# Kernel tuning notes

Measured on AMD Instinct MI355X. Metric: run time of the kernel, lower is better.

## Reference

```python
import jax, jax.numpy as jnp
import numpy as np
from math import sqrt

B, S, D, H = 2, 2048, 1024, 16
HD = D // H


def setup_inputs() -> dict:
    key = jax.random.key(0)
    ks = jax.random.split(key, 5)
    std = 0.02
    return {
        "tensor_in": jax.random.normal(ks[0], (B, S, D), dtype=jnp.float32),
        "attention_mask": jnp.zeros((1, 1, S, S), dtype=jnp.float32),
        "Wq": jax.random.normal(ks[1], (D, D), dtype=jnp.float32) * std,
        "Wk": jax.random.normal(ks[2], (D, D), dtype=jnp.float32) * std,
        "Wv": jax.random.normal(ks[3], (D, D), dtype=jnp.float32) * std,
        "Wo": jax.random.normal(ks[4], (D, D), dtype=jnp.float32) * std,
    }


def reference(tensor_in, attention_mask, Wq, Wk, Wv, Wo):
    # nn.Linear(dim, dim, bias=False): y = x @ W.T, W is [out, in]
    q = tensor_in @ Wq.T  # [B,S,D]
    k = tensor_in @ Wk.T
    v = tensor_in @ Wv.T
    # split heads -> [B,H,S,HD]
    q = q.reshape(B, S, H, HD).transpose(0, 2, 1, 3)
    k = k.reshape(B, S, H, HD).transpose(0, 2, 1, 3)
    v = v.reshape(B, S, H, HD).transpose(0, 2, 1, 3)
    # scores [B,H,S,S]; note: mask added BEFORE scaling, scale = sqrt(full dim)
    scores = jnp.einsum("bhqd,bhkd->bhqk", q, k) + attention_mask
    weights = jax.nn.softmax(scores / sqrt(D), axis=-1)  # dropout = identity (eval)
    context = jnp.einsum("bhqk,bhkd->bhqd", weights, v)
    context = context.transpose(0, 2, 1, 3).reshape(B, S, D)
    return context @ Wo.T
```

## Files before the change

kernel.cpp:

```cpp
#include <hip/hip_runtime.h>

#define B_  2
#define S_  2048
#define D_  1024
#define H_  16
#define HD_ 64
#define M_  (B_*S_)

typedef __attribute__((ext_vector_type(8))) short  short8;
typedef __attribute__((ext_vector_type(4))) float  float4v;
typedef __attribute__((ext_vector_type(4))) int    int4v;

#define PSCALE 0.0450843341f

__device__ __forceinline__ unsigned int pack2_bf16(float a, float b) {
#if __has_builtin(__builtin_amdgcn_cvt_pk_bf16_f32)
    auto p = __builtin_amdgcn_cvt_pk_bf16_f32(a, b);
    return __builtin_bit_cast(unsigned int, p);
#else
    unsigned int xa = __builtin_bit_cast(unsigned int, a);
    unsigned int xb = __builtin_bit_cast(unsigned int, b);
    xa += 0x7fffu + ((xa >> 16) & 1u);
    xb += 0x7fffu + ((xb >> 16) & 1u);
    return (xa >> 16) | (xb & 0xffff0000u);
#endif
}
__device__ __forceinline__ unsigned short f_to_bf16bits(float f) {
#if __has_builtin(__builtin_amdgcn_cvt_pk_bf16_f32)
    return (unsigned short)(pack2_bf16(f, f) & 0xffffu);
#else
    unsigned int x = __builtin_bit_cast(unsigned int, f);
    x += 0x7fffu + ((x >> 16) & 1u);
    return (unsigned short)(x >> 16);
#endif
}

__device__ __forceinline__ float fast_exp2(float x) {
#if __has_builtin(__builtin_amdgcn_exp2f)
    return __builtin_amdgcn_exp2f(x);
#else
    return exp2f(x);
#endif
}

__device__ __forceinline__ void async_cp16(const unsigned short* gsrc,
                                           unsigned short* lds_base_uniform) {
#if __has_builtin(__builtin_amdgcn_global_load_lds)
    __builtin_amdgcn_global_load_lds(
        (const __attribute__((address_space(1))) unsigned int*)gsrc,
        (__attribute__((address_space(3))) unsigned int*)lds_base_uniform,
        16, 0, 0);
#else
    const int lane = (int)(threadIdx.x & 63);
    *(int4v*)(lds_base_uniform + lane * 8) = *(const int4v*)gsrc;
#endif
}

__global__ __launch_bounds__(256) void cvt_bf16(
    const float* __restrict__ X,  const float* __restrict__ Wq,
    const float* __restrict__ Wk, const float* __restrict__ Wv,
    const float* __restrict__ Wo,
    unsigned short* __restrict__ Xb,  unsigned short* __restrict__ Wqb,
    unsigned short* __restrict__ Wkb, unsigned short* __restrict__ Wvb,
    unsigned short* __restrict__ Wob)
{
    const long t = (long)blockIdx.x * 256 + threadIdx.x;
    const long e = t * 8;
    const float* src; unsigned short* dst; long off;
    if      (e < 4194304) { src = X;  dst = Xb;  off = e; }
    else if (e < 5242880) { src = Wq; dst = Wqb; off = e - 4194304; }
    else if (e < 6291456) { src = Wk; dst = Wkb; off = e - 5242880; }
    else if (e < 7340032) { src = Wv; dst = Wvb; off = e - 6291456; }
    else                  { src = Wo; dst = Wob; off = e - 7340032; }
    float4v a = *(const float4v*)&src[off];
    float4v b = *(const float4v*)&src[off + 4];
    int4v o;
    o[0] = (int)pack2_bf16(a[0], a[1]);
    o[1] = (int)pack2_bf16(a[2], a[3]);
    o[2] = (int)pack2_bf16(b[0], b[1]);
    o[3] = (int)pack2_bf16(b[2], b[3]);
    *(int4v*)&dst[off] = o;
}

__global__ __launch_bounds__(256) void gemm_bt(
    const unsigned short* __restrict__ A,
    const unsigned short* __restrict__ B0,
    const unsigned short* __restrict__ B1,
    const unsigned short* __restrict__ B2,
    void* __restrict__ O0, void* __restrict__ O1, void* __restrict__ O2,
    int mode_base)
{
    const int K = 1024;
    const int z = blockIdx.z;
    const int mode = mode_base + z;
    const unsigned short* Aop;
    const unsigned short* Bop;
    void* Op = (z == 0) ? O0 : (z == 1) ? O1 : O2;
    int m0, n0;
    if (mode == 2) {
        Aop = B2; Bop = A;
        m0 = blockIdx.y * 128;
        n0 = blockIdx.x * 128;
    } else {
        Aop = A;
        Bop = (z == 0) ? B0 : (z == 1) ? B1 : B2;
        m0 = blockIdx.x * 128;
        n0 = blockIdx.y * 128;
    }

    __shared__ alignas(16) unsigned short As[128 * 64];
    __shared__ alignas(16) unsigned short Bs[128 * 64];

    const int tid  = threadIdx.x;
    const int wv   = tid >> 6;
    const int lane = tid & 63;
    const int wm   = wv >> 1, wn = wv & 1;
    const int q4   = lane >> 4, l15 = lane & 15;

    const unsigned short* gA[4];
    const unsigned short* gB[4];
    unsigned short* ldsA[4];
    unsigned short* ldsB[4];
#pragma unroll
    for (int j = 0; j < 4; j++) {
        const int r = wv * 32 + j * 8 + (lane >> 3);
        const int c = (((lane & 7) ^ (r & 7)) * 8);
        gA[j] = Aop + (long)(m0 + r) * K + c;
        gB[j] = Bop + (long)(n0 + r) * K + c;
        ldsA[j] = &As[(wv * 32 + j * 8) * 64];
        ldsB[j] = &Bs[(wv * 32 + j * 8) * 64];
    }

    int aoff[2][4], boff[2][4];
#pragma unroll
    for (int ks = 0; ks < 2; ks++)
#pragma unroll
        for (int t = 0; t < 4; t++) {
            const int swz = (((ks * 4 + q4) ^ (l15 & 7)) * 8);
            aoff[ks][t] = (wm * 64 + t * 16 + l15) * 64 + swz;
            boff[ks][t] = (wn * 64 + t * 16 + l15) * 64 + swz;
        }

    float4v acc[4][4];
#pragma unroll
    for (int i = 0; i < 4; i++)
#pragma unroll
        for (int j = 0; j < 4; j++) acc[i][j] = (float4v)0.0f;

    for (int k0 = 0; k0 < K; k0 += 64) {
        __syncthreads();
#pragma unroll
        for (int j = 0; j < 4; j++) {
            async_cp16(gA[j], ldsA[j]);
            async_cp16(gB[j], ldsB[j]);
            gA[j] += 64; gB[j] += 64;
        }
        __syncthreads();

#pragma unroll
        for (int ks = 0; ks < 2; ks++) {
            short8 afr[4], bfr[4];
#pragma unroll
            for (int mt = 0; mt < 4; mt++) afr[mt] = *(const short8*)&As[aoff[ks][mt]];
#pragma unroll
            for (int nt = 0; nt < 4; nt++) bfr[nt] = *(const short8*)&Bs[boff[ks][nt]];
#pragma unroll
            for (int mt = 0; mt < 4; mt++)
#pragma unroll
                for (int nt = 0; nt < 4; nt++)
                    acc[mt][nt] = __builtin_amdgcn_mfma_f32_16x16x32_bf16(
                        afr[mt], bfr[nt], acc[mt][nt], 0, 0, 0);
        }
    }

#pragma unroll
    for (int mt = 0; mt < 4; mt++)
#pragma unroll
        for (int nt = 0; nt < 4; nt++)
#pragma unroll
            for (int r = 0; r < 4; r++) {
                const int m = m0 + wm * 64 + mt * 16 + q4 * 4 + r;
                const int n = n0 + wn * 64 + nt * 16 + l15;
                float v = acc[mt][nt][r];
                if (mode == 3) {
                    ((float*)Op)[(long)m * D_ + n] = v;
                } else if (mode == 2) {
                    const long off = (((long)(n >> 11) * H_ + (m >> 6)) * HD_ + (m & 63)) * S_ + (n & 2047);
                    ((unsigned short*)Op)[off] = f_to_bf16bits(v);
                } else {
                    const long off = ((long)((m >> 11) * H_ + (n >> 6)) * S_ + (m & 2047)) * HD_ + (n & 63);
                    if (mode == 0) v *= PSCALE;
                    ((unsigned short*)Op)[off] = f_to_bf16bits(v);
                }
            }
}

__global__ __launch_bounds__(512, 4) void attn(
    const unsigned short* __restrict__ Q,
    const unsigned short* __restrict__ Kk,
    const unsigned short* __restrict__ Vt,
    const float* __restrict__ mask,
    unsigned short* __restrict__ ctx)
{
    __shared__ alignas(16) unsigned short Ks [2][64 * 72];
    __shared__ alignas(16) unsigned short Vts[2][64 * 72];
    __shared__ alignas(16) unsigned short Ps [8][16 * 72];

    const int tid  = threadIdx.x;
    const int wv   = tid >> 6;
    const int lane = tid & 63;
    const int q4   = lane >> 4, l15 = lane & 15;
    const int bh   = blockIdx.y;
    const int q0   = blockIdx.x * 128;

    const long head = (long)bh * S_ * HD_;

    const int qrow = q0 + wv * 16 + l15;
    short8 qfr[2];
    qfr[0] = *(const short8*)&Q[head + (long)qrow * HD_ + q4 * 8];
    qfr[1] = *(const short8*)&Q[head + (long)qrow * HD_ + 32 + q4 * 8];

    float l_acc[4] = {0.0f, 0.0f, 0.0f, 0.0f};
    float4v oacc[4];
#pragma unroll
    for (int dt = 0; dt < 4; dt++) oacc[dt] = (float4v)0.0f;

    const int srow = tid >> 3;
    const int scol = (tid & 7) * 8;
    const unsigned short* gK = Kk + head + (long)srow * HD_ + scol;
    const unsigned short* gV = Vt + head + (long)srow * S_  + scol;
    const int ldsOff = srow * 72 + scol;

    const float* mrow[4];
#pragma unroll
    for (int r = 0; r < 4; r++)
        mrow[r] = mask + (long)(q0 + wv * 16 + q4 * 4 + r) * S_ + l15;

    int4v kreg = *(const int4v*)gK;
    int4v vreg = *(const int4v*)gV;

    for (int it = 0; it < S_ / 64; it++) {
        const int k0  = it * 64;
        const int buf = it & 1;

        *(int4v*)&Ks [buf][ldsOff] = kreg;
        *(int4v*)&Vts[buf][ldsOff] = vreg;
        __syncthreads();

        if (it + 1 < S_ / 64) {
            kreg = *(const int4v*)(gK + (long)(k0 + 64) * HD_);
            vreg = *(const int4v*)(gV + (k0 + 64));
        }

        float mv[4][4];
#pragma unroll
        for (int nt = 0; nt < 4; nt++)
#pragma unroll
            for (int r = 0; r < 4; r++)
                mv[nt][r] = mrow[r][k0 + nt * 16];

        float4v sfr[4];
#pragma unroll
        for (int nt = 0; nt < 4; nt++) {
            short8 kb0 = *(const short8*)&Ks[buf][(nt * 16 + l15) * 72 + q4 * 8];
            short8 kb1 = *(const short8*)&Ks[buf][(nt * 16 + l15) * 72 + 32 + q4 * 8];
            float4v s = (float4v)0.0f;
            s = __builtin_amdgcn_mfma_f32_16x16x32_bf16(qfr[0], kb0, s, 0, 0, 0);
            s = __builtin_amdgcn_mfma_f32_16x16x32_bf16(qfr[1], kb1, s, 0, 0, 0);
            sfr[nt] = s;
        }

#pragma unroll
        for (int nt = 0; nt < 4; nt++)
#pragma unroll
            for (int r = 0; r < 4; r++) {
                const float p = fast_exp2(fmaf(mv[nt][r], PSCALE, sfr[nt][r]));
                l_acc[r] += p;
                Ps[wv][(q4 * 4 + r) * 72 + nt * 16 + l15] = f_to_bf16bits(p);
            }

        short8 pf0 = *(const short8*)&Ps[wv][l15 * 72 + q4 * 8];
        short8 pf1 = *(const short8*)&Ps[wv][l15 * 72 + 32 + q4 * 8];

#pragma unroll
        for (int dt = 0; dt < 4; dt++) {
            short8 vb0 = *(const short8*)&Vts[buf][(dt * 16 + l15) * 72 + q4 * 8];
            short8 vb1 = *(const short8*)&Vts[buf][(dt * 16 + l15) * 72 + 32 + q4 * 8];
            float4v o = oacc[dt];
            o = __builtin_amdgcn_mfma_f32_16x16x32_bf16(pf0, vb0, o, 0, 0, 0);
            o = __builtin_amdgcn_mfma_f32_16x16x32_bf16(pf1, vb1, o, 0, 0, 0);
            oacc[dt] = o;
        }
    }

#pragma unroll
    for (int r = 0; r < 4; r++) {
#pragma unroll
        for (int off = 1; off < 16; off <<= 1)
            l_acc[r] += __shfl_xor(l_acc[r], off);
    }

    const int b = bh >> 4, h = bh & 15;
#pragma unroll
    for (int dt = 0; dt < 4; dt++)
#pragma unroll
        for (int r = 0; r < 4; r++) {
            const int qg = q0 + wv * 16 + q4 * 4 + r;
            const int d  = dt * 16 + l15;
            const float v = oacc[dt][r] / l_acc[r];
            ctx[((long)(b * S_ + qg)) * D_ + h * HD_ + d] = f_to_bf16bits(v);
        }
}

extern "C" void kernel_launch(void* const* d_in, const int* in_sizes, int n_in,
                              void* d_out, int out_size, void* d_ws, size_t ws_size,
                              hipStream_t stream) {
    const float* X    = (const float*)d_in[0];
    const float* mask = (const float*)d_in[1];
    const float* Wq   = (const float*)d_in[2];
    const float* Wk   = (const float*)d_in[3];
    const float* Wv   = (const float*)d_in[4];
    const float* Wo   = (const float*)d_in[5];
    float* out        = (float*)d_out;

    unsigned short* ws = (unsigned short*)d_ws;
    unsigned short* qws  = ws;
    unsigned short* kws  = ws + 4194304;
    unsigned short* vtws = ws + 8388608;
    unsigned short* ctx  = ws + 12582912;
    unsigned short* Xb   = ws + 16777216;
    unsigned short* Wqb  = ws + 20971520;
    unsigned short* Wkb  = ws + 22020096;
    unsigned short* Wvb  = ws + 23068672;
    unsigned short* Wob  = ws + 24117248;

    cvt_bf16<<<dim3(4096), 256, 0, stream>>>(X, Wq, Wk, Wv, Wo, Xb, Wqb, Wkb, Wvb, Wob);
    gemm_bt<<<dim3(32, 8, 3), 256, 0, stream>>>(Xb, Wqb, Wkb, Wvb, qws, kws, vtws, 0);
    attn<<<dim3(16, 32, 1), 512, 0, stream>>>(qws, kws, vtws, mask, ctx);
    gemm_bt<<<dim3(32, 8, 1), 256, 0, stream>>>(ctx, Wob, Wob, Wob, out, out, out, 3);
}
```

Before: 222.9 us.

## Compute transposed scores and build P operand in registers via permlane swaps

Swaps the MFMA operand order so each lane holds four consecutive key columns of a single query row. This lets the P fragment for the PV MFMA be assembled in registers with permlane32/16 swaps instead of a round trip through shared memory, which removes the Ps LDS buffer and its writes and reads. Mask loads become vectorized float4 loads. The row-sum reduction becomes two cross-lane shuffles plus a broadcast, and launch bounds now request 8 waves per SIMD, which may force register spills.

Measured after the change: 249.3 us. 1.12x slower.

```diff
diff --git a/kernel.cpp b/kernel.cpp
--- a/kernel.cpp
+++ b/kernel.cpp
@@ -40,6 +40,25 @@
     return __builtin_amdgcn_exp2f(x);
 #else
     return exp2f(x);
+#endif
+}
+
+__device__ __forceinline__ void plswap(unsigned int a, unsigned int b,
+                                       unsigned int& lo, unsigned int& hi) {
+#if __has_builtin(__builtin_amdgcn_permlane32_swap) && __has_builtin(__builtin_amdgcn_permlane16_swap)
+    auto t = __builtin_amdgcn_permlane32_swap(a, b, false, false);
+    auto u = __builtin_amdgcn_permlane16_swap(t[0], t[1], false, false);
+    lo = u[0]; hi = u[1];
+#else
+    const int lane = (int)(threadIdx.x & 63);
+    unsigned int bx = __shfl_xor(b, 32);
+    unsigned int ax = __shfl_xor(a, 32);
+    unsigned int t0 = (lane & 32) ? bx : a;
+    unsigned int t1 = (lane & 32) ? b  : ax;
+    unsigned int t0x = __shfl_xor(t0, 16);
+    unsigned int t1x = __shfl_xor(t1, 16);
+    lo = (lane & 16) ? t1x : t0;
+    hi = (lane & 16) ? t1  : t0x;
 #endif
 }
 
@@ -195,7 +214,7 @@
             }
 }
 
-__global__ __launch_bounds__(512, 4) void attn(
+__global__ __launch_bounds__(512, 8) void attn(
     const unsigned short* __restrict__ Q,
     const unsigned short* __restrict__ Kk,
     const unsigned short* __restrict__ Vt,
@@ -204,7 +223,6 @@
 {
     __shared__ alignas(16) unsigned short Ks [2][64 * 72];
     __shared__ alignas(16) unsigned short Vts[2][64 * 72];
-    __shared__ alignas(16) unsigned short Ps [8][16 * 72];
 
     const int tid  = threadIdx.x;
     const int wv   = tid >> 6;
@@ -220,7 +238,7 @@
     qfr[0] = *(const short8*)&Q[head + (long)qrow * HD_ + q4 * 8];
     qfr[1] = *(const short8*)&Q[head + (long)qrow * HD_ + 32 + q4 * 8];
 
-    float l_acc[4] = {0.0f, 0.0f, 0.0f, 0.0f};
+    float l_acc = 0.0f;
     float4v oacc[4];
 #pragma unroll
     for (int dt = 0; dt < 4; dt++) oacc[dt] = (float4v)0.0f;
@@ -231,10 +249,7 @@
     const unsigned short* gV = Vt + head + (long)srow * S_  + scol;
     const int ldsOff = srow * 72 + scol;
 
-    const float* mrow[4];
-#pragma unroll
-    for (int r = 0; r < 4; r++)
-        mrow[r] = mask + (long)(q0 + wv * 16 + q4 * 4 + r) * S_ + l15;
+    const float* mrowp = mask + (long)qrow * S_ + q4 * 4;
 
     int4v kreg = *(const int4v*)gK;
     int4v vreg = *(const int4v*)gV;
@@ -252,12 +267,10 @@
             vreg = *(const int4v*)(gV + (k0 + 64));
         }
 
-        float mv[4][4];
+        float4v mv[4];
 #pragma unroll
         for (int nt = 0; nt < 4; nt++)
-#pragma unroll
-            for (int r = 0; r < 4; r++)
-                mv[nt][r] = mrow[r][k0 + nt * 16];
+            mv[nt] = *(const float4v*)(mrowp + k0 + nt * 16);
 
         float4v sfr[4];
 #pragma unroll
@@ -265,49 +278,59 @@
             short8 kb0 = *(const short8*)&Ks[buf][(nt * 16 + l15) * 72 + q4 * 8];
             short8 kb1 = *(const short8*)&Ks[buf][(nt * 16 + l15) * 72 + 32 + q4 * 8];
             float4v s = (float4v)0.0f;
-            s = __builtin_amdgcn_mfma_f32_16x16x32_bf16(qfr[0], kb0, s, 0, 0, 0);
-            s = __builtin_amdgcn_mfma_f32_16x16x32_bf16(qfr[1], kb1, s, 0, 0, 0);
+            s = __builtin_amdgcn_mfma_f32_16x16x32_bf16(kb0, qfr[0], s, 0, 0, 0);
+            s = __builtin_amdgcn_mfma_f32_16x16x32_bf16(kb1, qfr[1], s, 0, 0, 0);
             sfr[nt] = s;
         }
 
-#pragma unroll
-        for (int nt = 0; nt < 4; nt++)
-#pragma unroll
-            for (int r = 0; r < 4; r++) {
-                const float p = fast_exp2(fmaf(mv[nt][r], PSCALE, sfr[nt][r]));
-                l_acc[r] += p;
-                Ps[wv][(q4 * 4 + r) * 72 + nt * 16 + l15] = f_to_bf16bits(p);
-            }
-
-        short8 pf0 = *(const short8*)&Ps[wv][l15 * 72 + q4 * 8];
-        short8 pf1 = *(const short8*)&Ps[wv][l15 * 72 + 32 + q4 * 8];
+        unsigned int w[4][2];
+#pragma unroll
+        for (int nt = 0; nt < 4; nt++) {
+            float pv0 = fast_exp2(fmaf(mv[nt][0], PSCALE, sfr[nt][0]));
+            float pv1 = fast_exp2(fmaf(mv[nt][1], PSCALE, sfr[nt][1]));
+            float pv2 = fast_exp2(fmaf(mv[nt][2], PSCALE, sfr[nt][2]));
+            float pv3 = fast_exp2(fmaf(mv[nt][3], PSCALE, sfr[nt][3]));
+            l_acc += (pv0 + pv1) + (pv2 + pv3);
+            w[nt][0] = pack2_bf16(pv0, pv1);
+            w[nt][1] = pack2_bf16(pv2, pv3);
+        }
+        short8 pa[2];
+#pragma unroll
+        for (int kk = 0; kk < 2; kk++) {
+            unsigned int d0, d1, d2, d3;
+            plswap(w[2 * kk][0], w[2 * kk + 1][0], d0, d2);
+            plswap(w[2 * kk][1], w[2 * kk + 1][1], d1, d3);
+            int4v pw;
+            pw[0] = (int)d0; pw[1] = (int)d1; pw[2] = (int)d2; pw[3] = (int)d3;
+            pa[kk] = __builtin_bit_cast(short8, pw);
+        }
 
 #pragma unroll
         for (int dt = 0; dt < 4; dt++) {
             short8 vb0 = *(const short8*)&Vts[buf][(dt * 16 + l15) * 72 + q4 * 8];
             short8 vb1 = *(const short8*)&Vts[buf][(dt * 16 + l15) * 72 + 32 + q4 * 8];
             float4v o = oacc[dt];
-            o = __builtin_amdgcn_mfma_f32_16x16x32_bf16(pf0, vb0, o, 0, 0, 0);
-            o = __builtin_amdgcn_mfma_f32_16x16x32_bf16(pf1, vb1, o, 0, 0, 0);
+            o = __builtin_amdgcn_mfma_f32_16x16x32_bf16(pa[0], vb0, o, 0, 0, 0);
+            o = __builtin_amdgcn_mfma_f32_16x16x32_bf16(pa[1], vb1, o, 0, 0, 0);
             oacc[dt] = o;
         }
     }
 
-#pragma unroll
-    for (int r = 0; r < 4; r++) {
-#pragma unroll
-        for (int off = 1; off < 16; off <<= 1)
-            l_acc[r] += __shfl_xor(l_acc[r], off);
-    }
+    l_acc += __shfl_xor(l_acc, 16);
+    l_acc += __shfl_xor(l_acc, 32);
 
     const int b = bh >> 4, h = bh & 15;
+    float lr[4];
+#pragma unroll
+    for (int r = 0; r < 4; r++)
+        lr[r] = __shfl(l_acc, q4 * 4 + r, 16);
 #pragma unroll
     for (int dt = 0; dt < 4; dt++)
 #pragma unroll
         for (int r = 0; r < 4; r++) {
             const int qg = q0 + wv * 16 + q4 * 4 + r;
             const int d  = dt * 16 + l15;
-            const float v = oacc[dt][r] / l_acc[r];
+            const float v = oacc[dt][r] / lr[r];
             ctx[((long)(b * S_ + qg)) * D_ + h * HD_ + d] = f_to_bf16bits(v);
         }
 }
```
